# Kernel tuning notes

Measured on AMD Instinct MI355X. Metric: run time of the kernel, lower is better.

## Reference

```python
import jax, jax.numpy as jnp
import numpy as np

N_NODES = 50000
N_EDGES = 800000
D = 64
N_BASIS = 8


def setup_inputs() -> dict:
    key = jax.random.key(0)
    ks = jax.random.split(key, 16)
    inp = {
        "p": jax.random.normal(ks[0], (N_NODES, D), dtype=jnp.float32),
        "idx_i": jax.random.randint(ks[1], (N_EDGES,), 0, N_NODES),
        "idx_j": jax.random.randint(ks[2], (N_EDGES,), 0, N_NODES),
        "basis": jax.random.normal(ks[3], (N_EDGES, N_BASIS), dtype=jnp.float32),
        # pp_layer MLP: [64, 64, 64], activation tanh between layers
        "pp_W1": jax.random.normal(ks[4], (D, D), dtype=jnp.float32) / np.sqrt(D),
        "pp_b1": jnp.zeros((D,), dtype=jnp.float32),
        "pp_W2": jax.random.normal(ks[5], (D, D), dtype=jnp.float32) / np.sqrt(D),
        "pp_b2": jnp.zeros((D,), dtype=jnp.float32),
        # pi_layer MLP: n_neurons = [128, 64, 64, 64*8], activation=None, last layer no bias
        "pi_W1": jax.random.normal(ks[6], (2 * D, D), dtype=jnp.float32) / np.sqrt(2 * D),
        "pi_b1": jnp.zeros((D,), dtype=jnp.float32),
        "pi_W2": jax.random.normal(ks[7], (D, D), dtype=jnp.float32) / np.sqrt(D),
        "pi_b2": jnp.zeros((D,), dtype=jnp.float32),
        "pi_W3": jax.random.normal(ks[8], (D, D * N_BASIS), dtype=jnp.float32) / np.sqrt(D),
        # ii_layer MLP: [64, 64, 64], activation tanh between layers
        "ii_W1": jax.random.normal(ks[9], (D, D), dtype=jnp.float32) / np.sqrt(D),
        "ii_b1": jnp.zeros((D,), dtype=jnp.float32),
        "ii_W2": jax.random.normal(ks[10], (D, D), dtype=jnp.float32) / np.sqrt(D),
        "ii_b2": jnp.zeros((D,), dtype=jnp.float32),
    }
    return inp


def reference(p, idx_i, idx_j, basis,
              pp_W1, pp_b1, pp_W2, pp_b2,
              pi_W1, pi_b1, pi_W2, pi_b2, pi_W3,
              ii_W1, ii_b1, ii_W2, ii_b2):
    # pp_layer: node MLP (tanh between layers, no activation after last)
    p1 = jnp.tanh(p @ pp_W1 + pp_b1) @ pp_W2 + pp_b2          # [N, D]

    # PILayer: gather endpoint features, concat, linear MLP (activation=None), basis contraction
    inter = jnp.concatenate([p1[idx_i], p1[idx_j]], axis=-1)  # [E, 2D]
    inter = inter @ pi_W1 + pi_b1                              # [E, D]
    inter = inter @ pi_W2 + pi_b2                              # [E, D]
    inter = inter @ pi_W3                                      # [E, D*n_basis] (no bias)
    inter = inter.reshape(inter.shape[0], D, N_BASIS)          # [E, D, n_basis]
    i1 = jnp.einsum('ecb,eb->ec', inter, basis)                # [E, D]

    # ii_layer: edge MLP
    i1 = jnp.tanh(i1 @ ii_W1 + ii_b1) @ ii_W2 + ii_b2          # [E, D]

    # IPLayer: scatter_add edge features back to nodes (dim_size = p1.shape[0])
    out = jax.ops.segment_sum(i1, idx_j, num_segments=p1.shape[0])  # [N, D]
    return out
```

## Files before the change

kernel.cpp:

```cpp
#include <hip/hip_runtime.h>

#define N_NODES 50000
#define N_EDGES 800000
#define NPAD 50176

typedef float f32x4 __attribute__((ext_vector_type(4)));
typedef short bf16x8 __attribute__((ext_vector_type(8)));

__device__ __forceinline__ float fast_tanh(float x) {
  float e = __expf(2.0f * x);
  float r;
  asm("v_rcp_f32 %0, %1" : "=v"(r) : "v"(e + 1.0f));
  return fmaf(-2.0f, r, 1.0f);
}

__device__ __forceinline__ unsigned short f2bf_rne(float x) {
  unsigned u = __float_as_uint(x);
  unsigned r = u + 0x7FFFu + ((u >> 16) & 1u);
  return (unsigned short)(r >> 16);
}

__device__ __forceinline__ void packW(const float* __restrict__ W,
                                      unsigned short* __restrict__ dst, int tid) {
  int ks = tid >> 8, ct = (tid >> 6) & 3, lane = tid & 63;
  int k0 = ks * 32 + ((lane >> 4) << 3);
  int col = ct * 16 + (lane & 15);
  const float* src = W + k0 * 64 + col;
  unsigned u[4];
  #pragma unroll
  for (int jj = 0; jj < 4; ++jj) {
    float v0 = src[(2 * jj) * 64];
    float v1 = src[(2 * jj + 1) * 64];
    asm("v_cvt_pk_bf16_f32 %0, %1, %2" : "=v"(u[jj]) : "v"(v0), "v"(v1));
  }
  *(uint4*)(dst + (size_t)tid * 8) = make_uint4(u[0], u[1], u[2], u[3]);
}

__device__ __forceinline__ void mfma_gemm(const unsigned short* __restrict__ actIn,
                                          const unsigned short* __restrict__ bpk,
                                          int w, int l, f32x4 acc[4]) {
  int m = l & 15, s = l >> 4;
  int row = w * 16 + m;
  int sw = (m & 7) << 3;
  #pragma unroll
  for (int ks = 0; ks < 2; ++ks) {
    bf16x8 a = *(const bf16x8*)(actIn + row * 64 + ((ks * 32 + s * 8) ^ sw));
    #pragma unroll
    for (int ct = 0; ct < 4; ++ct) {
      bf16x8 b = *(const bf16x8*)(bpk + ((size_t)((ks * 4 + ct) * 64 + l)) * 8);
      acc[ct] = __builtin_amdgcn_mfma_f32_16x16x32_bf16(a, b, acc[ct], 0, 0, 0);
    }
  }
}

__device__ __forceinline__ void store_act(unsigned short* __restrict__ actOut,
                                          int w, int l, const f32x4 acc[4],
                                          bool do_tanh) {
  int m = l & 15, s = l >> 4;
  #pragma unroll
  for (int ct = 0; ct < 4; ++ct) {
    #pragma unroll
    for (int r = 0; r < 4; ++r) {
      int row = w * 16 + s * 4 + r;
      float v = acc[ct][r];
      if (do_tanh) v = fast_tanh(v);
      actOut[row * 64 + ((ct * 16 + m) ^ ((row & 7) << 3))] = f2bf_rne(v);
    }
  }
}

__global__ __launch_bounds__(512) void front_kernel(
    const float* __restrict__ p, const int* __restrict__ idx_j,
    const float* __restrict__ ppW1, const float* __restrict__ ppb1,
    const float* __restrict__ ppW2, const float* __restrict__ ppb2,
    const float* __restrict__ piW1, const float* __restrict__ pib1,
    const float* __restrict__ piW2, const float* __restrict__ pib2,
    const float* __restrict__ piW3, const float* __restrict__ iiW1,
    const float* __restrict__ iiW2,
    int* __restrict__ counts,
    float* __restrict__ qa, float* __restrict__ qb, float* __restrict__ b12,
    unsigned short* __restrict__ Bpack, unsigned short* __restrict__ W2pack) {
  int bid = blockIdx.x;
  int tid = threadIdx.x;

  if (bid >= 464) {
    int e = (bid - 464) * 512 + tid;
    if (e < N_EDGES) atomicAdd(&counts[idx_j[e]], 1);
    return;
  }
  if (bid >= 391) {
    int gid = (bid - 391) * 512 + tid;
    if (gid < 32768) {
      int j = gid & 7;
      int lane = (gid >> 3) & 63;
      int ct = (gid >> 9) & 3;
      int ks = gid >> 11;
      int kidx = ks * 32 + ((lane >> 4) << 3) + j;
      int col = ct * 16 + (lane & 15);
      int k = kidx >> 3, b = kidx & 7;
      float acc = 0.f;
      #pragma unroll 8
      for (int mm = 0; mm < 64; ++mm)
        acc = fmaf(piW3[k * 512 + mm * 8 + b], iiW1[mm * 64 + col], acc);
      Bpack[gid] = f2bf_rne(acc);
    } else if (gid < 32832) {
      int c = gid - 32768;
      float acc = pib2[c];
      for (int k = 0; k < 64; ++k) acc = fmaf(pib1[k], piW2[k * 64 + c], acc);
      b12[c] = acc;
    } else if (gid < 36928) {
      int g2 = gid - 32832;
      int j = g2 & 7;
      int lane = (g2 >> 3) & 63;
      int ct = (g2 >> 9) & 3;
      int ks = g2 >> 11;
      int kidx = ks * 32 + ((lane >> 4) << 3) + j;
      int col = ct * 16 + (lane & 15);
      W2pack[g2] = f2bf_rne(iiW2[kidx * 64 + col]);
    }
    return;
  }

  __shared__ __align__(16) unsigned short sBpk[2][4096];
  __shared__ __align__(16) unsigned short sAct[2][8192];

  int w = tid >> 6, l = tid & 63;
  int m = l & 15;
  int nb0 = bid * 128;

  for (int t = tid; t < 2048; t += 512) {
    int row = t >> 4, q = t & 15;
    int g = nb0 + row;
    float4 v = make_float4(0.f, 0.f, 0.f, 0.f);
    if (g < N_NODES) v = ((const float4*)p)[g * 16 + q];
    unsigned u0, u1;
    asm("v_cvt_pk_bf16_f32 %0, %1, %2" : "=v"(u0) : "v"(v.x), "v"(v.y));
    asm("v_cvt_pk_bf16_f32 %0, %1, %2" : "=v"(u1) : "v"(v.z), "v"(v.w));
    int sw = (row & 7) << 3;
    *(uint2*)(&sAct[0][row * 64 + ((q * 4) ^ sw)]) = make_uint2(u0, u1);
  }
  packW(ppW1, sBpk[0], tid);
  packW(ppW2, sBpk[1], tid);
  __syncthreads();

  f32x4 acc[4];
  #pragma unroll
  for (int ct = 0; ct < 4; ++ct) {
    float bv = ppb1[ct * 16 + m];
    acc[ct] = (f32x4){bv, bv, bv, bv};
  }
  mfma_gemm(sAct[0], sBpk[0], w, l, acc);
  store_act(sAct[1], w, l, acc, true);
  __syncthreads();

  #pragma unroll
  for (int ct = 0; ct < 4; ++ct) {
    float bv = ppb2[ct * 16 + m];
    acc[ct] = (f32x4){bv, bv, bv, bv};
  }
  mfma_gemm(sAct[1], sBpk[1], w, l, acc);
  store_act(sAct[0], w, l, acc, false);
  __syncthreads();

  packW(piW1, sBpk[0], tid);
  packW(piW2, sBpk[1], tid);
  __syncthreads();

  #pragma unroll
  for (int ct = 0; ct < 4; ++ct) acc[ct] = (f32x4){0.f, 0.f, 0.f, 0.f};
  mfma_gemm(sAct[0], sBpk[0], w, l, acc);
  store_act(sAct[1], w, l, acc, false);
  __syncthreads();

  #pragma unroll
  for (int ct = 0; ct < 4; ++ct) acc[ct] = (f32x4){0.f, 0.f, 0.f, 0.f};
  mfma_gemm(sAct[1], sBpk[1], w, l, acc);
  {
    int s = l >> 4;
    #pragma unroll
    for (int ct = 0; ct < 4; ++ct)
      #pragma unroll
      for (int r = 0; r < 4; ++r) {
        int rg = nb0 + w * 16 + s * 4 + r;
        if (rg < N_NODES) qa[(size_t)rg * 64 + ct * 16 + m] = acc[ct][r];
      }
  }
  packW(piW1 + 4096, sBpk[0], tid);
  __syncthreads();

  #pragma unroll
  for (int ct = 0; ct < 4; ++ct) acc[ct] = (f32x4){0.f, 0.f, 0.f, 0.f};
  mfma_gemm(sAct[0], sBpk[0], w, l, acc);
  store_act(sAct[1], w, l, acc, false);
  __syncthreads();

  #pragma unroll
  for (int ct = 0; ct < 4; ++ct) acc[ct] = (f32x4){0.f, 0.f, 0.f, 0.f};
  mfma_gemm(sAct[1], sBpk[1], w, l, acc);
  {
    int s = l >> 4;
    #pragma unroll
    for (int ct = 0; ct < 4; ++ct)
      #pragma unroll
      for (int r = 0; r < 4; ++r) {
        int rg = nb0 + w * 16 + s * 4 + r;
        if (rg < N_NODES) qb[(size_t)rg * 64 + ct * 16 + m] = acc[ct][r];
      }
  }
}

__global__ __launch_bounds__(1024) void scan_kernel(
    const int* __restrict__ counts, int* __restrict__ cursors) {
  __shared__ int buf[1024];
  __shared__ int red[16];
  int b = blockIdx.x, tid = threadIdx.x;
  int idx = b * 1024 + tid;
  int v = counts[idx];
  buf[tid] = v;
  int partial = 0;
  for (int i = tid; i < b * 1024; i += 1024) partial += counts[i];
  #pragma unroll
  for (int off = 32; off >= 1; off >>= 1) partial += __shfl_down(partial, off, 64);
  if ((tid & 63) == 0) red[tid >> 6] = partial;
  __syncthreads();
  for (int off = 1; off < 1024; off <<= 1) {
    int t = (tid >= off) ? buf[tid - off] : 0;
    __syncthreads();
    buf[tid] += t;
    __syncthreads();
  }
  int base = 0;
  #pragma unroll
  for (int i = 0; i < 16; ++i) base += red[i];
  cursors[idx] = base + buf[tid] - v;
}

__global__ __launch_bounds__(256) void sort_scatter_kernel(
    const int* __restrict__ idx_i, const int* __restrict__ idx_j,
    int* __restrict__ cursors,
    int2* __restrict__ sorted_ij, int* __restrict__ sorted_e) {
  int e = blockIdx.x * 256 + threadIdx.x;
  if (e < N_EDGES) {
    int j = idx_j[e];
    int pos = atomicAdd(&cursors[j], 1);
    sorted_ij[pos] = make_int2(idx_i[e], j);
    sorted_e[pos] = e;
  }
}

__global__ __launch_bounds__(1024, 8) void edge_kernel(
    const int2* __restrict__ sorted_ij, const int* __restrict__ sorted_e,
    const float* __restrict__ basis,
    const float* __restrict__ qa, const float* __restrict__ qb,
    const float* __restrict__ b12,
    const unsigned short* __restrict__ Bpack,
    const unsigned short* __restrict__ W2pack,
    const float* __restrict__ iib1, const float* __restrict__ iib2,
    float* __restrict__ out) {
  __shared__ __align__(16) unsigned short sB[32768];
  float* sH2 = (float*)sB;
  unsigned short* sT = sB;
  float* sF = (float*)sB;

  int tid = threadIdx.x;
  int e0 = blockIdx.x * 256;

  for (int t = tid; t < 4096; t += 1024) {
    int e = t >> 4, q = t & 15;
    int2 se = sorted_ij[e0 + e];
    float4 va = ((const float4*)qa)[se.x * 16 + q];
    float4 vb = ((const float4*)qb)[se.y * 16 + q];
    float4 vc = ((const float4*)b12)[q];
    float4 h;
    h.x = va.x + vb.x + vc.x;
    h.y = va.y + vb.y + vc.y;
    h.z = va.z + vb.z + vc.z;
    h.w = va.w + vb.w + vc.w;
    int dw = e * 64 + ((q * 4) ^ ((e & 7) << 3));
    *((float4*)(sH2 + dw)) = h;
  }
  __syncthreads();

  int w = tid >> 6, l = tid & 63;
  int m = l & 15, s = l >> 4;
  int eloc = w * 16 + m;
  int swz = (eloc & 7) << 3;

  float h2r[16];
  #pragma unroll
  for (int t = 0; t < 16; ++t) h2r[t] = sH2[eloc * 64 + ((t * 4 + s) ^ swz)];

  float bas[8];
  {
    int eorig = sorted_e[e0 + eloc];
    const float4* bp = (const float4*)(basis + (size_t)eorig * 8);
    float4 b0 = bp[0], b1 = bp[1];
    bas[0] = b0.x; bas[1] = b0.y; bas[2] = b0.z; bas[3] = b0.w;
    bas[4] = b1.x; bas[5] = b1.y; bas[6] = b1.z; bas[7] = b1.w;
  }
  __syncthreads();

  {
    const uint4* g = (const uint4*)Bpack;
    uint4* d = (uint4*)sB;
    #pragma unroll
    for (int t = 0; t < 4; ++t) d[tid + t * 1024] = g[tid + t * 1024];
  }
  __syncthreads();

  f32x4 c0, c1, c2, c3;
  {
    float v0 = iib1[m], v1 = iib1[16 + m], v2 = iib1[32 + m], v3 = iib1[48 + m];
    c0 = (f32x4){v0, v0, v0, v0};
    c1 = (f32x4){v1, v1, v1, v1};
    c2 = (f32x4){v2, v2, v2, v2};
    c3 = (f32x4){v3, v3, v3, v3};
  }

  const bf16x8* Bl = (const bf16x8*)sB;
  #pragma unroll
  for (int ks = 0; ks < 16; ++ks) {
    bf16x8 B0 = Bl[(ks * 4 + 0) * 64 + l];
    bf16x8 B1 = Bl[(ks * 4 + 1) * 64 + l];
    bf16x8 B2 = Bl[(ks * 4 + 2) * 64 + l];
    bf16x8 B3 = Bl[(ks * 4 + 3) * 64 + l];
    float hv = h2r[ks];
    union { unsigned u[4]; bf16x8 v; } A;
    #pragma unroll
    for (int j = 0; j < 4; ++j) {
      float p0 = hv * bas[2 * j];
      float p1 = hv * bas[2 * j + 1];
      asm("v_cvt_pk_bf16_f32 %0, %1, %2" : "=v"(A.u[j]) : "v"(p0), "v"(p1));
    }
    c0 = __builtin_amdgcn_mfma_f32_16x16x32_bf16(A.v, B0, c0, 0, 0, 0);
    c1 = __builtin_amdgcn_mfma_f32_16x16x32_bf16(A.v, B1, c1, 0, 0, 0);
    c2 = __builtin_amdgcn_mfma_f32_16x16x32_bf16(A.v, B2, c2, 0, 0, 0);
    c3 = __builtin_amdgcn_mfma_f32_16x16x32_bf16(A.v, B3, c3, 0, 0, 0);
  }
  __syncthreads();

  #pragma unroll
  for (int r = 0; r < 4; ++r) {
    int row = w * 16 + s * 4 + r;
    sT[row * 72 + 0 * 16 + m] = f2bf_rne(fast_tanh(c0[r]));
    sT[row * 72 + 1 * 16 + m] = f2bf_rne(fast_tanh(c1[r]));
    sT[row * 72 + 2 * 16 + m] = f2bf_rne(fast_tanh(c2[r]));
    sT[row * 72 + 3 * 16 + m] = f2bf_rne(fast_tanh(c3[r]));
  }
  __syncthreads();

  f32x4 d0, d1, d2, d3;
  {
    float v0 = iib2[m], v1 = iib2[16 + m], v2 = iib2[32 + m], v3 = iib2[48 + m];
    d0 = (f32x4){v0, v0, v0, v0};
    d1 = (f32x4){v1, v1, v1, v1};
    d2 = (f32x4){v2, v2, v2, v2};
    d3 = (f32x4){v3, v3, v3, v3};
  }
  const bf16x8* Wl = (const bf16x8*)W2pack;
  #pragma unroll
  for (int ks = 0; ks < 2; ++ks) {
    bf16x8 Af = *(const bf16x8*)(sT + eloc * 72 + ks * 32 + s * 8);
    d0 = __builtin_amdgcn_mfma_f32_16x16x32_bf16(Af, Wl[(ks * 4 + 0) * 64 + l], d0, 0, 0, 0);
    d1 = __builtin_amdgcn_mfma_f32_16x16x32_bf16(Af, Wl[(ks * 4 + 1) * 64 + l], d1, 0, 0, 0);
    d2 = __builtin_amdgcn_mfma_f32_16x16x32_bf16(Af, Wl[(ks * 4 + 2) * 64 + l], d2, 0, 0, 0);
    d3 = __builtin_amdgcn_mfma_f32_16x16x32_bf16(Af, Wl[(ks * 4 + 3) * 64 + l], d3, 0, 0, 0);
  }

  #pragma unroll
  for (int h = 0; h < 2; ++h) {
    __syncthreads();
    if ((w >> 3) == h) {
      int wl = w & 7;
      #pragma unroll
      for (int r = 0; r < 4; ++r) {
        int row = wl * 16 + s * 4 + r;
        sF[row * 68 + 0  + m] = d0[r];
        sF[row * 68 + 16 + m] = d1[r];
        sF[row * 68 + 32 + m] = d2[r];
        sF[row * 68 + 48 + m] = d3[r];
      }
    }
    __syncthreads();
    {
      int base_e = e0 + h * 128 + w * 8;
      float acc = sF[(w * 8) * 68 + l];
      int cur_j = sorted_ij[base_e].y;
      #pragma unroll
      for (int rr = 1; rr < 8; ++rr) {
        int nj = sorted_ij[base_e + rr].y;
        float v = sF[(w * 8 + rr) * 68 + l];
        if (nj == cur_j) {
          acc += v;
        } else {
          atomicAdd(&out[(size_t)cur_j * 64 + l], acc);
          acc = v;
          cur_j = nj;
        }
      }
      atomicAdd(&out[(size_t)cur_j * 64 + l], acc);
    }
  }
}

extern "C" void kernel_launch(void* const* d_in, const int* in_sizes, int n_in,
                              void* d_out, int out_size, void* d_ws, size_t ws_size,
                              hipStream_t stream) {
  const float* p     = (const float*)d_in[0];
  const int*   idx_i = (const int*)d_in[1];
  const int*   idx_j = (const int*)d_in[2];
  const float* basis = (const float*)d_in[3];
  const float* ppW1  = (const float*)d_in[4];
  const float* ppb1  = (const float*)d_in[5];
  const float* ppW2  = (const float*)d_in[6];
  const float* ppb2  = (const float*)d_in[7];
  const float* piW1  = (const float*)d_in[8];
  const float* pib1  = (const float*)d_in[9];
  const float* piW2  = (const float*)d_in[10];
  const float* pib2  = (const float*)d_in[11];
  const float* piW3  = (const float*)d_in[12];
  const float* iiW1  = (const float*)d_in[13];
  const float* iib1  = (const float*)d_in[14];
  const float* iiW2  = (const float*)d_in[15];
  const float* iib2  = (const float*)d_in[16];

  float* ws  = (float*)d_ws;
  float* qa  = ws;
  float* qb  = ws + 3200000;
  float* b12 = ws + 6400000;
  unsigned short* Bpack  = (unsigned short*)(ws + 6400064);
  unsigned short* W2pack = (unsigned short*)(ws + 6416448);
  int* counts    = (int*)(ws + 6418496);
  int* cursors   = (int*)(ws + 6468672);
  int2* sorted_ij = (int2*)(ws + 6518848);
  int* sorted_e   = (int*)(ws + 8118848);

  hipMemsetAsync(d_out, 0, (size_t)out_size * sizeof(float), stream);
  hipMemsetAsync(counts, 0, (size_t)NPAD * sizeof(int), stream);
  front_kernel<<<2027, 512, 0, stream>>>(p, idx_j, ppW1, ppb1, ppW2, ppb2,
                                         piW1, pib1, piW2, pib2, piW3, iiW1, iiW2,
                                         counts, qa, qb, b12, Bpack, W2pack);
  scan_kernel<<<49, 1024, 0, stream>>>(counts, cursors);
  sort_scatter_kernel<<<3125, 256, 0, stream>>>(idx_i, idx_j, cursors,
                                                sorted_ij, sorted_e);
  edge_kernel<<<3125, 1024, 0, stream>>>(sorted_ij, sorted_e, basis,
                                         qa, qb, b12, Bpack, W2pack,
                                         iib1, iib2, (float*)d_out);
}
```

Baseline: 252.0 us.

## Regroup kernels so node MLP overlaps sort scatter, prefetch edge loads early

```diff
diff --git a/kernel.cpp b/kernel.cpp
--- a/kernel.cpp
+++ b/kernel.cpp
@@ -69,54 +69,97 @@
   }
 }
 
-__global__ __launch_bounds__(512) void front_kernel(
-    const float* __restrict__ p, const int* __restrict__ idx_j,
-    const float* __restrict__ ppW1, const float* __restrict__ ppb1,
-    const float* __restrict__ ppW2, const float* __restrict__ ppb2,
-    const float* __restrict__ piW1, const float* __restrict__ pib1,
-    const float* __restrict__ piW2, const float* __restrict__ pib2,
+__global__ __launch_bounds__(512) void hist_prep_kernel(
+    const int* __restrict__ idx_j,
+    const float* __restrict__ piW2, const float* __restrict__ pib1,
+    const float* __restrict__ pib2,
     const float* __restrict__ piW3, const float* __restrict__ iiW1,
     const float* __restrict__ iiW2,
-    int* __restrict__ counts,
-    float* __restrict__ qa, float* __restrict__ qb, float* __restrict__ b12,
+    int* __restrict__ counts, float* __restrict__ b12,
     unsigned short* __restrict__ Bpack, unsigned short* __restrict__ W2pack) {
   int bid = blockIdx.x;
   int tid = threadIdx.x;
-
-  if (bid >= 464) {
-    int e = (bid - 464) * 512 + tid;
+  if (bid < 1563) {
+    int e = bid * 512 + tid;
     if (e < N_EDGES) atomicAdd(&counts[idx_j[e]], 1);
     return;
   }
+  int gid = (bid - 1563) * 512 + tid;
+  if (gid < 32768) {
+    int j = gid & 7;
+    int lane = (gid >> 3) & 63;
+    int ct = (gid >> 9) & 3;
+    int ks = gid >> 11;
+    int kidx = ks * 32 + ((lane >> 4) << 3) + j;
+    int col = ct * 16 + (lane & 15);
+    int k = kidx >> 3, b = kidx & 7;
+    float acc = 0.f;
+    #pragma unroll 8
+    for (int mm = 0; mm < 64; ++mm)
+      acc = fmaf(piW3[k * 512 + mm * 8 + b], iiW1[mm * 64 + col], acc);
+    Bpack[gid] = f2bf_rne(acc);
+  } else if (gid < 32832) {
+    int c = gid - 32768;
+    float acc = pib2[c];
+    for (int k = 0; k < 64; ++k) acc = fmaf(pib1[k], piW2[k * 64 + c], acc);
+    b12[c] = acc;
+  } else if (gid < 36928) {
+    int g2 = gid - 32832;
+    int j = g2 & 7;
+    int lane = (g2 >> 3) & 63;
+    int ct = (g2 >> 9) & 3;
+    int ks = g2 >> 11;
+    int kidx = ks * 32 + ((lane >> 4) << 3) + j;
+    int col = ct * 16 + (lane & 15);
+    W2pack[g2] = f2bf_rne(iiW2[kidx * 64 + col]);
+  }
+}
+
+__global__ __launch_bounds__(1024) void scan_kernel(
+    const int* __restrict__ counts, int* __restrict__ cursors) {
+  __shared__ int buf[1024];
+  __shared__ int red[16];
+  int b = blockIdx.x, tid = threadIdx.x;
+  int idx = b * 1024 + tid;
+  int v = counts[idx];
+  buf[tid] = v;
+  int partial = 0;
+  for (int i = tid; i < b * 1024; i += 1024) partial += counts[i];
+  #pragma unroll
+  for (int off = 32; off >= 1; off >>= 1) partial += __shfl_down(partial, off, 64);
+  if ((tid & 63) == 0) red[tid >> 6] = partial;
+  __syncthreads();
+  for (int off = 1; off < 1024; off <<= 1) {
+    int t = (tid >= off) ? buf[tid - off] : 0;
+    __syncthreads();
+    buf[tid] += t;
+    __syncthreads();
+  }
+  int base = 0;
+  #pragma unroll
+  for (int i = 0; i < 16; ++i) base += red[i];
+  cursors[idx] = base + buf[tid] - v;
+}
+
+__global__ __launch_bounds__(512) void node_scatter_kernel(
+    const float* __restrict__ p,
+    const int* __restrict__ idx_i, const int* __restrict__ idx_j,
+    const float* __restrict__ ppW1, const float* __restrict__ ppb1,
+    const float* __restrict__ ppW2, const float* __restrict__ ppb2,
+    const float* __restrict__ piW1, const float* __restrict__ piW2,
+    int* __restrict__ cursors,
+    float* __restrict__ qa, float* __restrict__ qb,
+    int2* __restrict__ sorted_ij, int* __restrict__ sorted_e) {
+  int bid = blockIdx.x;
+  int tid = threadIdx.x;
+
   if (bid >= 391) {
-    int gid = (bid - 391) * 512 + tid;
-    if (gid < 32768) {
-      int j = gid & 7;
-      int lane = (gid >> 3) & 63;
-      int ct = (gid >> 9) & 3;
-      int ks = gid >> 11;
-      int kidx = ks * 32 + ((lane >> 4) << 3) + j;
-      int col = ct * 16 + (lane & 15);
-      int k = kidx >> 3, b = kidx & 7;
-      float acc = 0.f;
-      #pragma unroll 8
-      for (int mm = 0; mm < 64; ++mm)
-        acc = fmaf(piW3[k * 512 + mm * 8 + b], iiW1[mm * 64 + col], acc);
-      Bpack[gid] = f2bf_rne(acc);
-    } else if (gid < 32832) {
-      int c = gid - 32768;
-      float acc = pib2[c];
-      for (int k = 0; k < 64; ++k) acc = fmaf(pib1[k], piW2[k * 64 + c], acc);
-      b12[c] = acc;
-    } else if (gid < 36928) {
-      int g2 = gid - 32832;
-      int j = g2 & 7;
-      int lane = (g2 >> 3) & 63;
-      int ct = (g2 >> 9) & 3;
-      int ks = g2 >> 11;
-      int kidx = ks * 32 + ((lane >> 4) << 3) + j;
-      int col = ct * 16 + (lane & 15);
-      W2pack[g2] = f2bf_rne(iiW2[kidx * 64 + col]);
+    int e = (bid - 391) * 512 + tid;
+    if (e < N_EDGES) {
+      int j = idx_j[e];
+      int pos = atomicAdd(&cursors[j], 1);
+      sorted_ij[pos] = make_int2(idx_i[e], j);
+      sorted_e[pos] = e;
     }
     return;
   }
@@ -206,45 +249,6 @@
         int rg = nb0 + w * 16 + s * 4 + r;
         if (rg < N_NODES) qb[(size_t)rg * 64 + ct * 16 + m] = acc[ct][r];
       }
-  }
-}
-
-__global__ __launch_bounds__(1024) void scan_kernel(
-    const int* __restrict__ counts, int* __restrict__ cursors) {
-  __shared__ int buf[1024];
-  __shared__ int red[16];
-  int b = blockIdx.x, tid = threadIdx.x;
-  int idx = b * 1024 + tid;
-  int v = counts[idx];
-  buf[tid] = v;
-  int partial = 0;
-  for (int i = tid; i < b * 1024; i += 1024) partial += counts[i];
-  #pragma unroll
-  for (int off = 32; off >= 1; off >>= 1) partial += __shfl_down(partial, off, 64);
-  if ((tid & 63) == 0) red[tid >> 6] = partial;
-  __syncthreads();
-  for (int off = 1; off < 1024; off <<= 1) {
-    int t = (tid >= off) ? buf[tid - off] : 0;
-    __syncthreads();
-    buf[tid] += t;
-    __syncthreads();
-  }
-  int base = 0;
-  #pragma unroll
-  for (int i = 0; i < 16; ++i) base += red[i];
-  cursors[idx] = base + buf[tid] - v;
-}
-
-__global__ __launch_bounds__(256) void sort_scatter_kernel(
-    const int* __restrict__ idx_i, const int* __restrict__ idx_j,
-    int* __restrict__ cursors,
-    int2* __restrict__ sorted_ij, int* __restrict__ sorted_e) {
-  int e = blockIdx.x * 256 + threadIdx.x;
-  if (e < N_EDGES) {
-    int j = idx_j[e];
-    int pos = atomicAdd(&cursors[j], 1);
-    sorted_ij[pos] = make_int2(idx_i[e], j);
-    sorted_e[pos] = e;
   }
 }
 
@@ -264,6 +268,20 @@
 
   int tid = threadIdx.x;
   int e0 = blockIdx.x * 256;
+  int w = tid >> 6, l = tid & 63;
+  int m = l & 15, s = l >> 4;
+  int eloc = w * 16 + m;
+  int swz = (eloc & 7) << 3;
+
+  const uint4* gB = (const uint4*)Bpack;
+  uint4 bp0 = gB[tid];
+  uint4 bp1 = gB[tid + 1024];
+  uint4 bp2 = gB[tid + 2048];
+  uint4 bp3 = gB[tid + 3072];
+  int eorig = sorted_e[e0 + eloc];
+  const float4* bpt = (const float4*)(basis + (size_t)eorig * 8);
+  float4 bas01 = bpt[0];
+  float4 bas23 = bpt[1];
 
   for (int t = tid; t < 4096; t += 1024) {
     int e = t >> 4, q = t & 15;
@@ -281,30 +299,21 @@
   }
   __syncthreads();
 
-  int w = tid >> 6, l = tid & 63;
-  int m = l & 15, s = l >> 4;
-  int eloc = w * 16 + m;
-  int swz = (eloc & 7) << 3;
-
   float h2r[16];
   #pragma unroll
   for (int t = 0; t < 16; ++t) h2r[t] = sH2[eloc * 64 + ((t * 4 + s) ^ swz)];
 
   float bas[8];
+  bas[0] = bas01.x; bas[1] = bas01.y; bas[2] = bas01.z; bas[3] = bas01.w;
+  bas[4] = bas23.x; bas[5] = bas23.y; bas[6] = bas23.z; bas[7] = bas23.w;
+  __syncthreads();
+
   {
-    int eorig = sorted_e[e0 + eloc];
-    const float4* bp = (const float4*)(basis + (size_t)eorig * 8);
-    float4 b0 = bp[0], b1 = bp[1];
-    bas[0] = b0.x; bas[1] = b0.y; bas[2] = b0.z; bas[3] = b0.w;
-    bas[4] = b1.x; bas[5] = b1.y; bas[6] = b1.z; bas[7] = b1.w;
-  }
-  __syncthreads();
-
-  {
-    const uint4* g = (const uint4*)Bpack;
     uint4* d = (uint4*)sB;
-    #pragma unroll
-    for (int t = 0; t < 4; ++t) d[tid + t * 1024] = g[tid + t * 1024];
+    d[tid] = bp0;
+    d[tid + 1024] = bp1;
+    d[tid + 2048] = bp2;
+    d[tid + 3072] = bp3;
   }
   __syncthreads();
 
@@ -437,12 +446,14 @@
 
   hipMemsetAsync(d_out, 0, (size_t)out_size * sizeof(float), stream);
   hipMemsetAsync(counts, 0, (size_t)NPAD * sizeof(int), stream);
-  front_kernel<<<2027, 512, 0, stream>>>(p, idx_j, ppW1, ppb1, ppW2, ppb2,
-                                         piW1, pib1, piW2, pib2, piW3, iiW1, iiW2,
-                                         counts, qa, qb, b12, Bpack, W2pack);
+  hist_prep_kernel<<<1636, 512, 0, stream>>>(idx_j, piW2, pib1, pib2,
+                                             piW3, iiW1, iiW2,
+                                             counts, b12, Bpack, W2pack);
   scan_kernel<<<49, 1024, 0, stream>>>(counts, cursors);
-  sort_scatter_kernel<<<3125, 256, 0, stream>>>(idx_i, idx_j, cursors,
-                                                sorted_ij, sorted_e);
+  node_scatter_kernel<<<1954, 512, 0, stream>>>(p, idx_i, idx_j,
+                                                ppW1, ppb1, ppW2, ppb2,
+                                                piW1, piW2, cursors,
+                                                qa, qb, sorted_ij, sorted_e);
   edge_kernel<<<3125, 1024, 0, stream>>>(sorted_ij, sorted_e, basis,
                                          qa, qb, b12, Bpack, W2pack,
                                          iib1, iib2, (float*)d_out);
```

Result: faster. 245.7 us (-2.5%).
